# Optimization experiments

Hardware: AMD Instinct MI355X
Metric: run time of the kernel (lower is better)

The kernel has to match this reference:

```python
import jax, jax.numpy as jnp
import numpy as np

DIM_Q = 512
DIM_K = 512
DIM_V = 512
NUM_HEADS = 8
TEMPERATURE = 0.1
LN_EPS = 1e-5


def setup_inputs() -> dict:
    key = jax.random.key(0)
    ks = jax.random.split(key, 12)
    B, n_q, n_k = 8, 1024, 1024
    s = 0.02
    return {
        "Q": jax.random.normal(ks[0], (B, n_q, DIM_Q), jnp.float32),
        "K": jax.random.normal(ks[1], (B, n_k, DIM_K), jnp.float32),
        "mask": jnp.ones((B, n_k), dtype=bool),
        "Wq": jax.random.normal(ks[2], (DIM_Q, DIM_V), jnp.float32) * s,
        "bq": jnp.zeros((DIM_V,), jnp.float32),
        "Wk": jax.random.normal(ks[3], (DIM_K, DIM_V), jnp.float32) * s,
        "bk": jnp.zeros((DIM_V,), jnp.float32),
        "Wv": jax.random.normal(ks[4], (DIM_K, DIM_V), jnp.float32) * s,
        "bv": jnp.zeros((DIM_V,), jnp.float32),
        "Wo": jax.random.normal(ks[5], (DIM_V, DIM_V), jnp.float32) * s,
        "bo": jnp.zeros((DIM_V,), jnp.float32),
        "gamma": jnp.ones((DIM_V,), jnp.float32),
        "beta": jnp.zeros((DIM_V,), jnp.float32),
    }


def _mab(Q, K, mask, Wq, bq, Wk, bk, Wv, bv, Wo, bo, gamma, beta):
    B, n_q, _ = Q.shape
    n_k = K.shape[1]
    H = NUM_HEADS
    d_head = DIM_V // H
    # projections, split heads: [B, H, n, d_head]
    Qh = (Q @ Wq + bq).reshape(B, n_q, H, d_head).transpose(0, 2, 1, 3)
    Kh = (K @ Wk + bk).reshape(B, n_k, H, d_head).transpose(0, 2, 1, 3)
    Vh = (K @ Wv + bv).reshape(B, n_k, H, d_head).transpose(0, 2, 1, 3)
    scale = 1.0 / (np.sqrt(d_head) * TEMPERATURE)
    A = jnp.einsum("bhqd,bhkd->bhqk", Qh, Kh) * scale
    A = jnp.where(mask[:, None, None, :], A, -jnp.inf)
    A = jax.nn.softmax(A, axis=-1)
    O = jnp.einsum("bhqk,bhkd->bhqd", A, Vh)
    O = O.transpose(0, 2, 1, 3).reshape(B, n_q, DIM_V)
    # fused output FFN + residual + LN
    O = O + jax.nn.relu(O @ Wo + bo)
    mu = jnp.mean(O, axis=-1, keepdims=True)
    var = jnp.var(O, axis=-1, keepdims=True)
    return (O - mu) * jax.lax.rsqrt(var + LN_EPS) * gamma + beta


def reference(Q, K, mask, Wq, bq, Wk, bk, Wv, bv, Wo, bo, gamma, beta):
    return _mab(Q, K, mask, Wq, bq, Wk, bk, Wv, bv, Wo, bo, gamma, beta)
```

## Files before the change

### kernel.cpp

```cpp
#include <hip/hip_runtime.h>

typedef __bf16 bf16;
typedef bf16 bf16x4 __attribute__((ext_vector_type(4)));
typedef bf16 bf16x8 __attribute__((ext_vector_type(8)));
typedef float floatx4 __attribute__((ext_vector_type(4)));

#define NB 8
#define NQ 1024
#define NK 1024
#define DIM 512
#define NH 8
#define DH 64

__device__ __forceinline__ void async16(const void* g, void* l) {
    __builtin_amdgcn_global_load_lds(
        (const __attribute__((address_space(1))) unsigned int*)(unsigned long long)(g),
        (__attribute__((address_space(3))) unsigned int*)(unsigned long long)(l),
        16, 0, 0);
}

__global__ __launch_bounds__(256) void prep_fused(
    const float* __restrict__ Q, const float* __restrict__ K,
    const float* __restrict__ Wq, const float* __restrict__ Wk,
    const float* __restrict__ Wv, const float* __restrict__ Wo,
    bf16* __restrict__ Qb, bf16* __restrict__ Kb, bf16* __restrict__ Wt)
{
    __shared__ bf16 Tl[64][68];
    const int bid = blockIdx.x;
    if (bid < 4096) {
        const int i = bid * 256 + threadIdx.x;
        float4 a = ((const float4*)Q)[i];
        float4 c = ((const float4*)K)[i];
        bf16x4 qa = {(bf16)a.x, (bf16)a.y, (bf16)a.z, (bf16)a.w};
        bf16x4 ka = {(bf16)c.x, (bf16)c.y, (bf16)c.z, (bf16)c.w};
        *(bf16x4*)(Qb + (size_t)i * 4) = qa;
        *(bf16x4*)(Kb + (size_t)i * 4) = ka;
    } else {
        const int bid2 = bid - 4096;
        const int w = bid2 >> 6;
        const int bx = bid2 & 7, by = (bid2 >> 3) & 7;
        const float* W = (w == 0) ? Wq : (w == 1) ? Wk : (w == 2) ? Wv : Wo;
        bf16* out = Wt + (size_t)w * DIM * DIM;
        const int k0 = bx * 64, n0 = by * 64;
        const int tx = threadIdx.x & 15, ty = threadIdx.x >> 4;
        for (int pass = 0; pass < 4; ++pass) {
            int k = ty + pass * 16;
            float4 v = *(const float4*)&W[(size_t)(k0 + k) * DIM + n0 + tx * 4];
            Tl[tx * 4 + 0][k] = (bf16)v.x;
            Tl[tx * 4 + 1][k] = (bf16)v.y;
            Tl[tx * 4 + 2][k] = (bf16)v.z;
            Tl[tx * 4 + 3][k] = (bf16)v.w;
        }
        __syncthreads();
        for (int pass = 0; pass < 4; ++pass) {
            int n = ty + pass * 16;
            bf16x4 ov = *(const bf16x4*)&Tl[n][tx * 4];
            *(bf16x4*)&out[(size_t)(n0 + n) * DIM + k0 + tx * 4] = ov;
        }
    }
}

__global__ __launch_bounds__(256) void proj_fused(
    const bf16* __restrict__ Qb, const bf16* __restrict__ Kb,
    const bf16* __restrict__ Wt,
    const float* __restrict__ bq, const float* __restrict__ bk,
    const float* __restrict__ bv,
    bf16* __restrict__ Qp, bf16* __restrict__ Kp, bf16* __restrict__ Vpt)
{
    __shared__ __attribute__((aligned(16))) bf16 sh[16384];
    bf16* As = sh;
    bf16* Bs = sh + 8192;
    const int t = threadIdx.x;
    const int wave = t >> 6, lane = t & 63, quad = lane >> 4, l16 = lane & 15;
    const int wr = wave >> 1, wc = wave & 1;
    const int bid = blockIdx.x;
    const bool isQ = bid < 256;
    const bf16* A; const bf16* W; int m0, n0;
    if (isQ) { A = Qb; W = Wt;             m0 = (bid & 63) * 128;  n0 = (bid >> 6) * 128; }
    else     { int b2 = bid - 256;
               A = Kb; W = Wt + 512 * DIM; m0 = (b2 & 63) * 128;   n0 = (b2 >> 6) * 128; }

    const int r1 = t >> 3, s1 = t & 7;
    const int p1 = s1 ^ (r1 & 7);
    const bf16* aSrc = A + (size_t)(m0 + r1) * DIM + p1 * 8;
    const bf16* wSrc = W + (size_t)(n0 + r1) * DIM + p1 * 8;

    floatx4 acc[4][4];
    for (int i = 0; i < 4; ++i)
        for (int j = 0; j < 4; ++j) acc[i][j] = (floatx4){0.f, 0.f, 0.f, 0.f};

    for (int kt = 0; kt < 8; ++kt) {
        __syncthreads();
        const int ko = kt * 64;
        #pragma unroll
        for (int j = 0; j < 4; ++j) {
            async16(aSrc + ko + (size_t)j * 32 * DIM, As + (t + j * 256) * 8);
            async16(wSrc + ko + (size_t)j * 32 * DIM, Bs + (t + j * 256) * 8);
        }
        __syncthreads();
        #pragma unroll
        for (int ks = 0; ks < 2; ++ks) {
            bf16x8 af[4], bfr[4];
            #pragma unroll
            for (int mi = 0; mi < 4; ++mi) {
                const int row = wr * 64 + mi * 16 + l16;
                af[mi] = *(const bf16x8*)(As + row * 64 + (((ks * 4 + quad) ^ (row & 7)) << 3));
            }
            #pragma unroll
            for (int ni = 0; ni < 4; ++ni) {
                const int row = wc * 64 + ni * 16 + l16;
                bfr[ni] = *(const bf16x8*)(Bs + row * 64 + (((ks * 4 + quad) ^ (row & 7)) << 3));
            }
            #pragma unroll
            for (int mi = 0; mi < 4; ++mi)
                #pragma unroll
                for (int ni = 0; ni < 4; ++ni)
                    acc[mi][ni] = __builtin_amdgcn_mfma_f32_16x16x32_bf16(
                        af[mi], bfr[ni], acc[mi][ni], 0, 0, 0);
        }
    }

    const bool isV = (!isQ) && (n0 >= 512);
    if (!isV) {
        bf16* out = isQ ? Qp : Kp;
        const float* bias = isQ ? bq : bk;
        for (int ni = 0; ni < 4; ++ni) {
            const int n = n0 + wc * 64 + ni * 16 + l16;
            const float bb = bias[n];
            const int hd = n >> 6, d = n & 63;
            for (int mi = 0; mi < 4; ++mi) {
                for (int r = 0; r < 4; ++r) {
                    const int m = m0 + wr * 64 + mi * 16 + quad * 4 + r;
                    const int b = m >> 10, q = m & 1023;
                    out[((size_t)(b * 8 + hd) * 1024 + q) * 64 + d] = (bf16)(acc[mi][ni][r] + bb);
                }
            }
        }
    } else {
        __syncthreads();
        for (int ni = 0; ni < 4; ++ni) {
            const int n = wc * 64 + ni * 16 + l16;
            const float bb = bv[n0 + n - 512];
            for (int mi = 0; mi < 4; ++mi) {
                const int mb = wr * 64 + mi * 16 + quad * 4;
                const int slot = ((mb >> 3) ^ (n & 15));
                bf16x4 pk = {(bf16)(acc[mi][ni][0] + bb), (bf16)(acc[mi][ni][1] + bb),
                             (bf16)(acc[mi][ni][2] + bb), (bf16)(acc[mi][ni][3] + bb)};
                *(bf16x4*)(sh + n * 128 + slot * 8 + (mb & 7)) = pk;
            }
        }
        __syncthreads();
        const int n = t >> 1, hf = t & 1;
        const int nv = n0 + n - 512, hd = nv >> 6, d = nv & 63;
        const int b = m0 >> 10, qb = m0 & 1023;
        bf16* dst = Vpt + ((size_t)(b * 8 + hd) * 64 + d) * 1024 + qb + hf * 64;
        #pragma unroll
        for (int j = 0; j < 8; ++j) {
            const int ch = hf * 8 + j;
            const int slot = ch ^ (n & 15);
            bf16x8 v8 = *(const bf16x8*)(sh + n * 128 + slot * 8);
            *(bf16x8*)(dst + j * 8) = v8;
        }
    }
}

__global__ __launch_bounds__(256) void attn_kernel(
    const bf16* __restrict__ Qp, const bf16* __restrict__ Kp,
    const bf16* __restrict__ Vpt, const int* __restrict__ mask,
    bf16* __restrict__ Oa)
{
    const int bh = blockIdx.x & 63, qblk = blockIdx.x >> 6;
    const int b = bh >> 3, hd = bh & 7;
    const int t = threadIdx.x;
    const int wave = t >> 6, lane = t & 63, quad = lane >> 4, l16 = lane & 15;
    const float scale2 = 1.8033688011112042f;

    __shared__ __attribute__((aligned(16))) bf16 Kt[64 * 64];
    __shared__ __attribute__((aligned(16))) bf16 Vt[64 * 64];
    __shared__ __attribute__((aligned(16))) bf16 Pl[4][16 * 64];

    const bf16* Qbase = Qp + ((size_t)bh * NQ + qblk * 64 + wave * 16) * DH;
    const bf16* Kbase = Kp + (size_t)bh * NK * DH;
    const bf16* Vbase = Vpt + (size_t)bh * DH * NK;
    const int* mrow = mask + b * NK;

    bf16x8 qf[2];
    for (int hh = 0; hh < 2; ++hh)
        qf[hh] = *(const bf16x8*)(Qbase + l16 * DH + hh * 32 + quad * 8);

    floatx4 o[4];
    float lsum = 0.f;
    for (int i = 0; i < 4; ++i) o[i] = (floatx4){0.f, 0.f, 0.f, 0.f};

    const int r1 = t >> 3, s1 = t & 7;
    const int p1 = s1 ^ (r1 & 7);
    const bf16* kSrc = Kbase + r1 * 64 + p1 * 8;
    const bf16* vSrc = Vbase + (size_t)r1 * 1024 + p1 * 8;
    bf16* kDst0 = Kt + t * 8;
    bf16* kDst1 = Kt + (t + 256) * 8;
    bf16* vDst0 = Vt + t * 8;
    bf16* vDst1 = Vt + (t + 256) * 8;

    for (int kt = 0; kt < NK / 64; ++kt) {
        __syncthreads();
        async16(kSrc + kt * 4096, kDst0);
        async16(kSrc + kt * 4096 + 32 * 64, kDst1);
        async16(vSrc + kt * 64, vDst0);
        async16(vSrc + kt * 64 + (size_t)32 * 1024, vDst1);
        __syncthreads();

        bf16x8 kb[4][2];
        #pragma unroll
        for (int sub = 0; sub < 4; ++sub) {
            const int rowk = sub * 16 + l16;
            kb[sub][0] = *(const bf16x8*)(Kt + rowk * 64 + ((quad ^ (rowk & 7)) << 3));
            kb[sub][1] = *(const bf16x8*)(Kt + rowk * 64 + (((quad + 4) ^ (rowk & 7)) << 3));
        }
        floatx4 sf[4];
        #pragma unroll
        for (int sub = 0; sub < 4; ++sub) {
            floatx4 s = {0.f, 0.f, 0.f, 0.f};
            s = __builtin_amdgcn_mfma_f32_16x16x32_bf16(kb[sub][0], qf[0], s, 0, 0, 0);
            s = __builtin_amdgcn_mfma_f32_16x16x32_bf16(kb[sub][1], qf[1], s, 0, 0, 0);
            sf[sub] = s;
        }
        #pragma unroll
        for (int sub = 0; sub < 4; ++sub) {
            const int4 m4 = *(const int4*)&mrow[kt * 64 + sub * 16 + quad * 4];
            const float md0 = m4.x ? 0.f : -3.0e38f;
            const float md1 = m4.y ? 0.f : -3.0e38f;
            const float md2 = m4.z ? 0.f : -3.0e38f;
            const float md3 = m4.w ? 0.f : -3.0e38f;
            float p0 = exp2f(fmaf(sf[sub][0], scale2, md0));
            float p1v = exp2f(fmaf(sf[sub][1], scale2, md1));
            float p2 = exp2f(fmaf(sf[sub][2], scale2, md2));
            float p3 = exp2f(fmaf(sf[sub][3], scale2, md3));
            sf[sub][0] = p0; sf[sub][1] = p1v; sf[sub][2] = p2; sf[sub][3] = p3;
            lsum += p0 + p1v + p2 + p3;
        }
        #pragma unroll
        for (int sub = 0; sub < 4; ++sub) {
            bf16x4 pk = {(bf16)sf[sub][0], (bf16)sf[sub][1],
                         (bf16)sf[sub][2], (bf16)sf[sub][3]};
            const int p = sub * 2 + (quad >> 1);
            const int slot = p ^ (l16 & 7);
            *(bf16x4*)&Pl[wave][l16 * 64 + slot * 8 + (quad & 1) * 4] = pk;
        }
        bf16x8 af[2];
        #pragma unroll
        for (int hh = 0; hh < 2; ++hh) {
            const int p = hh * 4 + quad;
            const int slot = p ^ (l16 & 7);
            af[hh] = *(const bf16x8*)&Pl[wave][l16 * 64 + slot * 8];
        }
        #pragma unroll
        for (int dsub = 0; dsub < 4; ++dsub) {
            const int rowd = dsub * 16 + l16;
            bf16x8 v0 = *(const bf16x8*)(Vt + rowd * 64 + ((quad ^ (rowd & 7)) << 3));
            bf16x8 v1 = *(const bf16x8*)(Vt + rowd * 64 + (((quad + 4) ^ (rowd & 7)) << 3));
            o[dsub] = __builtin_amdgcn_mfma_f32_16x16x32_bf16(af[0], v0, o[dsub], 0, 0, 0);
            o[dsub] = __builtin_amdgcn_mfma_f32_16x16x32_bf16(af[1], v1, o[dsub], 0, 0, 0);
        }
    }

    float lr = lsum;
    lr += __shfl_xor(lr, 16, 64);
    lr += __shfl_xor(lr, 32, 64);
    const float inv = 1.f / lr;
    float linv[4];
    for (int r = 0; r < 4; ++r) linv[r] = __shfl(inv, quad * 4 + r, 64);
    for (int dsub = 0; dsub < 4; ++dsub) {
        for (int r = 0; r < 4; ++r) {
            const int q = qblk * 64 + wave * 16 + quad * 4 + r;
            const int col = hd * 64 + dsub * 16 + l16;
            Oa[((size_t)(b * NQ + q)) * DIM + col] = (bf16)(o[dsub][r] * linv[r]);
        }
    }
}

__global__ __launch_bounds__(256) void ffn_ln(
    const bf16* __restrict__ Oa, const bf16* __restrict__ W,
    const float* __restrict__ bo, const float* __restrict__ gamma,
    const float* __restrict__ beta, float* __restrict__ out)
{
    __shared__ __attribute__((aligned(16))) bf16 As[32 * 512];
    __shared__ __attribute__((aligned(16))) bf16 Bs[512 * 32];
    const int t = threadIdx.x;
    const int wave = t >> 6, lane = t & 63, quad = lane >> 4, l16 = lane & 15;
    const int m0 = blockIdx.x * 32;

    #pragma unroll
    for (int j = 0; j < 8; ++j) {
        const int c = t + j * 256;
        const int row = c >> 6, slot = c & 63;
        const int p = (slot & 56) | ((slot & 7) ^ (row & 7));
        async16(Oa + (size_t)(m0 + row) * DIM + p * 8, As + row * 512 + slot * 8);
    }

    floatx4 acc[2][8];
    for (int i = 0; i < 2; ++i)
        for (int j = 0; j < 8; ++j) acc[i][j] = (floatx4){0.f, 0.f, 0.f, 0.f};

    for (int kt = 0; kt < 16; ++kt) {
        __syncthreads();
        #pragma unroll
        for (int j = 0; j < 8; ++j) {
            const int c = t + j * 256;
            const int n = c >> 2, slot = c & 3;
            const int p = slot ^ ((n >> 1) & 3);
            async16(W + (size_t)n * DIM + kt * 32 + p * 8, Bs + n * 32 + slot * 8);
        }
        __syncthreads();
        bf16x8 af[2], bfr[8];
        #pragma unroll
        for (int mi = 0; mi < 2; ++mi) {
            const int row = mi * 16 + l16;
            const int part = kt * 4 + quad;
            const int slot = (part & 56) | ((part & 7) ^ (row & 7));
            af[mi] = *(const bf16x8*)(As + row * 512 + slot * 8);
        }
        #pragma unroll
        for (int ni = 0; ni < 8; ++ni) {
            const int n = wave * 128 + ni * 16 + l16;
            const int slot = quad ^ ((n >> 1) & 3);
            bfr[ni] = *(const bf16x8*)(Bs + n * 32 + slot * 8);
        }
        #pragma unroll
        for (int mi = 0; mi < 2; ++mi)
            #pragma unroll
            for (int ni = 0; ni < 8; ++ni)
                acc[mi][ni] = __builtin_amdgcn_mfma_f32_16x16x32_bf16(
                    af[mi], bfr[ni], acc[mi][ni], 0, 0, 0);
    }

    #pragma unroll
    for (int ni = 0; ni < 8; ++ni) {
        const int n = wave * 128 + ni * 16 + l16;
        const float bb = bo[n];
        const int part = n >> 3, noff = n & 7;
        #pragma unroll
        for (int mi = 0; mi < 2; ++mi) {
            #pragma unroll
            for (int r = 0; r < 4; ++r) {
                const int row = mi * 16 + quad * 4 + r;
                const int slot = (part & 56) | ((part & 7) ^ (row & 7));
                const float res = (float)As[row * 512 + slot * 8 + noff];
                acc[mi][ni][r] = res + fmaxf(acc[mi][ni][r] + bb, 0.f);
            }
        }
    }

    __syncthreads();
    float* Sm  = (float*)Bs;
    float* Sq  = Sm + 128;
    float* Mu  = Sm + 256;
    float* Inv = Sm + 288;
    #pragma unroll
    for (int mi = 0; mi < 2; ++mi) {
        #pragma unroll
        for (int r = 0; r < 4; ++r) {
            float s = 0.f, q2 = 0.f;
            #pragma unroll
            for (int ni = 0; ni < 8; ++ni) {
                const float v = acc[mi][ni][r];
                s += v; q2 += v * v;
            }
            s  += __shfl_xor(s, 1, 64);  q2 += __shfl_xor(q2, 1, 64);
            s  += __shfl_xor(s, 2, 64);  q2 += __shfl_xor(q2, 2, 64);
            s  += __shfl_xor(s, 4, 64);  q2 += __shfl_xor(q2, 4, 64);
            s  += __shfl_xor(s, 8, 64);  q2 += __shfl_xor(q2, 8, 64);
            if (l16 == 0) {
                const int row = mi * 16 + quad * 4 + r;
                Sm[wave * 32 + row] = s;
                Sq[wave * 32 + row] = q2;
            }
        }
    }
    __syncthreads();
    if (t < 32) {
        const float s  = Sm[t] + Sm[32 + t] + Sm[64 + t] + Sm[96 + t];
        const float q2 = Sq[t] + Sq[32 + t] + Sq[64 + t] + Sq[96 + t];
        const float mu = s * (1.f / 512.f);
        const float var = q2 * (1.f / 512.f) - mu * mu;
        Mu[t] = mu;
        Inv[t] = rsqrtf(var + 1e-5f);
    }
    __syncthreads();

    #pragma unroll
    for (int ni = 0; ni < 8; ++ni) {
        const int n = wave * 128 + ni * 16 + l16;
        const float gv = gamma[n], btv = beta[n];
        #pragma unroll
        for (int mi = 0; mi < 2; ++mi) {
            #pragma unroll
            for (int r = 0; r < 4; ++r) {
                const int row = mi * 16 + quad * 4 + r;
                const float mu = Mu[row], iv = Inv[row];
                out[(size_t)(m0 + row) * DIM + n] =
                    (acc[mi][ni][r] - mu) * iv * gv + btv;
            }
        }
    }
}

extern "C" void kernel_launch(void* const* d_in, const int* in_sizes, int n_in,
                              void* d_out, int out_size, void* d_ws, size_t ws_size,
                              hipStream_t stream) {
    const float* Q  = (const float*)d_in[0];
    const float* K  = (const float*)d_in[1];
    const int*   mask = (const int*)d_in[2];
    const float* Wq = (const float*)d_in[3];
    const float* bq = (const float*)d_in[4];
    const float* Wk = (const float*)d_in[5];
    const float* bk = (const float*)d_in[6];
    const float* Wv = (const float*)d_in[7];
    const float* bv = (const float*)d_in[8];
    const float* Wo = (const float*)d_in[9];
    const float* bo = (const float*)d_in[10];
    const float* gamma = (const float*)d_in[11];
    const float* beta  = (const float*)d_in[12];

    char* ws = (char*)d_ws;
    bf16* Wt  = (bf16*)(ws);
    bf16* Qb  = (bf16*)(ws + 2097152);
    bf16* Kb  = (bf16*)(ws + 10485760);
    bf16* Qp  = (bf16*)(ws + 18874368);
    bf16* Kp  = (bf16*)(ws + 27262976);
    bf16* Vpt = (bf16*)(ws + 35651584);
    bf16* Oa  = (bf16*)(ws + 44040192);
    float* out = (float*)d_out;

    prep_fused<<<4352, 256, 0, stream>>>(Q, K, Wq, Wk, Wv, Wo, Qb, Kb, Wt);
    proj_fused<<<768, 256, 0, stream>>>(Qb, Kb, Wt, bq, bk, bv, Qp, Kp, Vpt);
    attn_kernel<<<1024, 256, 0, stream>>>(Qp, Kp, Vpt, mask, Oa);
    ffn_ln<<<256, 256, 0, stream>>>(Oa, Wt + 3 * 262144, bo, gamma, beta, out);
}
```

Baseline: 186.9 us.

## Give attention waves two query groups each and halve FFN row tile

The attention kernel now runs 2 waves per block instead of 4. Each wave handles two 16-row query groups, so every K and V fragment loaded from LDS feeds twice as many MFMAs, and exp2 with a prescale is replaced by __expf with scale 1.25. The FFN+LayerNorm kernel processes 16 rows per block instead of 32, doubling the grid to 512 blocks for better occupancy. The tradeoffs are more registers per attention wave and more redundant reloads of Wo per row in the FFN.

```diff
diff --git a/kernel.cpp b/kernel.cpp
--- a/kernel.cpp
+++ b/kernel.cpp
@@ -164,7 +164,7 @@
     }
 }
 
-__global__ __launch_bounds__(256) void attn_kernel(
+__global__ __launch_bounds__(128) void attn_kernel(
     const bf16* __restrict__ Qp, const bf16* __restrict__ Kp,
     const bf16* __restrict__ Vpt, const int* __restrict__ mask,
     bf16* __restrict__ Oa)
@@ -173,40 +173,41 @@
     const int b = bh >> 3, hd = bh & 7;
     const int t = threadIdx.x;
     const int wave = t >> 6, lane = t & 63, quad = lane >> 4, l16 = lane & 15;
-    const float scale2 = 1.8033688011112042f;
+    const float scale = 1.25f;
 
     __shared__ __attribute__((aligned(16))) bf16 Kt[64 * 64];
     __shared__ __attribute__((aligned(16))) bf16 Vt[64 * 64];
-    __shared__ __attribute__((aligned(16))) bf16 Pl[4][16 * 64];
-
-    const bf16* Qbase = Qp + ((size_t)bh * NQ + qblk * 64 + wave * 16) * DH;
+    __shared__ __attribute__((aligned(16))) bf16 Pl[2][32 * 64];
+
+    const bf16* Qbase = Qp + ((size_t)bh * NQ + qblk * 64 + wave * 32) * DH;
     const bf16* Kbase = Kp + (size_t)bh * NK * DH;
     const bf16* Vbase = Vpt + (size_t)bh * DH * NK;
     const int* mrow = mask + b * NK;
 
-    bf16x8 qf[2];
-    for (int hh = 0; hh < 2; ++hh)
-        qf[hh] = *(const bf16x8*)(Qbase + l16 * DH + hh * 32 + quad * 8);
-
-    floatx4 o[4];
-    float lsum = 0.f;
-    for (int i = 0; i < 4; ++i) o[i] = (floatx4){0.f, 0.f, 0.f, 0.f};
+    bf16x8 qf[2][2];
+    for (int g = 0; g < 2; ++g)
+        for (int hh = 0; hh < 2; ++hh)
+            qf[g][hh] = *(const bf16x8*)(Qbase + (g * 16 + l16) * DH + hh * 32 + quad * 8);
+
+    floatx4 o[2][4];
+    float lsum[2];
+    for (int g = 0; g < 2; ++g) {
+        lsum[g] = 0.f;
+        for (int i = 0; i < 4; ++i) o[g][i] = (floatx4){0.f, 0.f, 0.f, 0.f};
+    }
 
     const int r1 = t >> 3, s1 = t & 7;
     const int p1 = s1 ^ (r1 & 7);
     const bf16* kSrc = Kbase + r1 * 64 + p1 * 8;
     const bf16* vSrc = Vbase + (size_t)r1 * 1024 + p1 * 8;
-    bf16* kDst0 = Kt + t * 8;
-    bf16* kDst1 = Kt + (t + 256) * 8;
-    bf16* vDst0 = Vt + t * 8;
-    bf16* vDst1 = Vt + (t + 256) * 8;
 
     for (int kt = 0; kt < NK / 64; ++kt) {
         __syncthreads();
-        async16(kSrc + kt * 4096, kDst0);
-        async16(kSrc + kt * 4096 + 32 * 64, kDst1);
-        async16(vSrc + kt * 64, vDst0);
-        async16(vSrc + kt * 64 + (size_t)32 * 1024, vDst1);
+        #pragma unroll
+        for (int j = 0; j < 4; ++j) {
+            async16(kSrc + kt * 4096 + j * 16 * 64, Kt + (t + j * 128) * 8);
+            async16(vSrc + kt * 64 + (size_t)j * 16 * 1024, Vt + (t + j * 128) * 8);
+        }
         __syncthreads();
 
         bf16x8 kb[4][2];
@@ -216,14 +217,16 @@
             kb[sub][0] = *(const bf16x8*)(Kt + rowk * 64 + ((quad ^ (rowk & 7)) << 3));
             kb[sub][1] = *(const bf16x8*)(Kt + rowk * 64 + (((quad + 4) ^ (rowk & 7)) << 3));
         }
-        floatx4 sf[4];
-        #pragma unroll
-        for (int sub = 0; sub < 4; ++sub) {
-            floatx4 s = {0.f, 0.f, 0.f, 0.f};
-            s = __builtin_amdgcn_mfma_f32_16x16x32_bf16(kb[sub][0], qf[0], s, 0, 0, 0);
-            s = __builtin_amdgcn_mfma_f32_16x16x32_bf16(kb[sub][1], qf[1], s, 0, 0, 0);
-            sf[sub] = s;
-        }
+        floatx4 sf[2][4];
+        #pragma unroll
+        for (int g = 0; g < 2; ++g)
+            #pragma unroll
+            for (int sub = 0; sub < 4; ++sub) {
+                floatx4 s = {0.f, 0.f, 0.f, 0.f};
+                s = __builtin_amdgcn_mfma_f32_16x16x32_bf16(kb[sub][0], qf[g][0], s, 0, 0, 0);
+                s = __builtin_amdgcn_mfma_f32_16x16x32_bf16(kb[sub][1], qf[g][1], s, 0, 0, 0);
+                sf[g][sub] = s;
+            }
         #pragma unroll
         for (int sub = 0; sub < 4; ++sub) {
             const int4 m4 = *(const int4*)&mrow[kt * 64 + sub * 16 + quad * 4];
@@ -231,49 +234,60 @@
             const float md1 = m4.y ? 0.f : -3.0e38f;
             const float md2 = m4.z ? 0.f : -3.0e38f;
             const float md3 = m4.w ? 0.f : -3.0e38f;
-            float p0 = exp2f(fmaf(sf[sub][0], scale2, md0));
-            float p1v = exp2f(fmaf(sf[sub][1], scale2, md1));
-            float p2 = exp2f(fmaf(sf[sub][2], scale2, md2));
-            float p3 = exp2f(fmaf(sf[sub][3], scale2, md3));
-            sf[sub][0] = p0; sf[sub][1] = p1v; sf[sub][2] = p2; sf[sub][3] = p3;
-            lsum += p0 + p1v + p2 + p3;
-        }
-        #pragma unroll
-        for (int sub = 0; sub < 4; ++sub) {
-            bf16x4 pk = {(bf16)sf[sub][0], (bf16)sf[sub][1],
-                         (bf16)sf[sub][2], (bf16)sf[sub][3]};
-            const int p = sub * 2 + (quad >> 1);
-            const int slot = p ^ (l16 & 7);
-            *(bf16x4*)&Pl[wave][l16 * 64 + slot * 8 + (quad & 1) * 4] = pk;
-        }
-        bf16x8 af[2];
-        #pragma unroll
-        for (int hh = 0; hh < 2; ++hh) {
-            const int p = hh * 4 + quad;
-            const int slot = p ^ (l16 & 7);
-            af[hh] = *(const bf16x8*)&Pl[wave][l16 * 64 + slot * 8];
-        }
+            #pragma unroll
+            for (int g = 0; g < 2; ++g) {
+                float p0 = __expf(sf[g][sub][0] * scale + md0);
+                float p1v = __expf(sf[g][sub][1] * scale + md1);
+                float p2 = __expf(sf[g][sub][2] * scale + md2);
+                float p3 = __expf(sf[g][sub][3] * scale + md3);
+                sf[g][sub][0] = p0; sf[g][sub][1] = p1v;
+                sf[g][sub][2] = p2; sf[g][sub][3] = p3;
+                lsum[g] += p0 + p1v + p2 + p3;
+            }
+        }
+        #pragma unroll
+        for (int g = 0; g < 2; ++g)
+            #pragma unroll
+            for (int sub = 0; sub < 4; ++sub) {
+                bf16x4 pk = {(bf16)sf[g][sub][0], (bf16)sf[g][sub][1],
+                             (bf16)sf[g][sub][2], (bf16)sf[g][sub][3]};
+                const int slot = (sub * 2 + (quad >> 1)) ^ (l16 & 7);
+                *(bf16x4*)&Pl[wave][(g * 16 + l16) * 64 + slot * 8 + (quad & 1) * 4] = pk;
+            }
+        bf16x8 af[2][2];
+        #pragma unroll
+        for (int g = 0; g < 2; ++g)
+            #pragma unroll
+            for (int hh = 0; hh < 2; ++hh) {
+                const int slot = (hh * 4 + quad) ^ (l16 & 7);
+                af[g][hh] = *(const bf16x8*)&Pl[wave][(g * 16 + l16) * 64 + slot * 8];
+            }
         #pragma unroll
         for (int dsub = 0; dsub < 4; ++dsub) {
             const int rowd = dsub * 16 + l16;
             bf16x8 v0 = *(const bf16x8*)(Vt + rowd * 64 + ((quad ^ (rowd & 7)) << 3));
             bf16x8 v1 = *(const bf16x8*)(Vt + rowd * 64 + (((quad + 4) ^ (rowd & 7)) << 3));
-            o[dsub] = __builtin_amdgcn_mfma_f32_16x16x32_bf16(af[0], v0, o[dsub], 0, 0, 0);
-            o[dsub] = __builtin_amdgcn_mfma_f32_16x16x32_bf16(af[1], v1, o[dsub], 0, 0, 0);
-        }
-    }
-
-    float lr = lsum;
-    lr += __shfl_xor(lr, 16, 64);
-    lr += __shfl_xor(lr, 32, 64);
-    const float inv = 1.f / lr;
-    float linv[4];
-    for (int r = 0; r < 4; ++r) linv[r] = __shfl(inv, quad * 4 + r, 64);
-    for (int dsub = 0; dsub < 4; ++dsub) {
-        for (int r = 0; r < 4; ++r) {
-            const int q = qblk * 64 + wave * 16 + quad * 4 + r;
-            const int col = hd * 64 + dsub * 16 + l16;
-            Oa[((size_t)(b * NQ + q)) * DIM + col] = (bf16)(o[dsub][r] * linv[r]);
+            #pragma unroll
+            for (int g = 0; g < 2; ++g) {
+                o[g][dsub] = __builtin_amdgcn_mfma_f32_16x16x32_bf16(af[g][0], v0, o[g][dsub], 0, 0, 0);
+                o[g][dsub] = __builtin_amdgcn_mfma_f32_16x16x32_bf16(af[g][1], v1, o[g][dsub], 0, 0, 0);
+            }
+        }
+    }
+
+    for (int g = 0; g < 2; ++g) {
+        float lr = lsum[g];
+        lr += __shfl_xor(lr, 16, 64);
+        lr += __shfl_xor(lr, 32, 64);
+        const float inv = 1.f / lr;
+        float linv[4];
+        for (int r = 0; r < 4; ++r) linv[r] = __shfl(inv, quad * 4 + r, 64);
+        for (int dsub = 0; dsub < 4; ++dsub) {
+            for (int r = 0; r < 4; ++r) {
+                const int q = qblk * 64 + wave * 32 + g * 16 + quad * 4 + r;
+                const int col = hd * 64 + dsub * 16 + l16;
+                Oa[((size_t)(b * NQ + q)) * DIM + col] = (bf16)(o[g][dsub][r] * linv[r]);
+            }
         }
     }
 }
@@ -283,23 +297,22 @@
     const float* __restrict__ bo, const float* __restrict__ gamma,
     const float* __restrict__ beta, float* __restrict__ out)
 {
-    __shared__ __attribute__((aligned(16))) bf16 As[32 * 512];
+    __shared__ __attribute__((aligned(16))) bf16 As[16 * 512];
     __shared__ __attribute__((aligned(16))) bf16 Bs[512 * 32];
     const int t = threadIdx.x;
     const int wave = t >> 6, lane = t & 63, quad = lane >> 4, l16 = lane & 15;
-    const int m0 = blockIdx.x * 32;
+    const int m0 = blockIdx.x * 16;
 
     #pragma unroll
-    for (int j = 0; j < 8; ++j) {
+    for (int j = 0; j < 4; ++j) {
         const int c = t + j * 256;
         const int row = c >> 6, slot = c & 63;
         const int p = (slot & 56) | ((slot & 7) ^ (row & 7));
         async16(Oa + (size_t)(m0 + row) * DIM + p * 8, As + row * 512 + slot * 8);
     }
 
-    floatx4 acc[2][8];
-    for (int i = 0; i < 2; ++i)
-        for (int j = 0; j < 8; ++j) acc[i][j] = (floatx4){0.f, 0.f, 0.f, 0.f};
+    floatx4 acc[8];
+    for (int j = 0; j < 8; ++j) acc[j] = (floatx4){0.f, 0.f, 0.f, 0.f};
 
     for (int kt = 0; kt < 16; ++kt) {
         __syncthreads();
@@ -311,13 +324,11 @@
             async16(W + (size_t)n * DIM + kt * 32 + p * 8, Bs + n * 32 + slot * 8);
         }
         __syncthreads();
-        bf16x8 af[2], bfr[8];
-        #pragma unroll
-        for (int mi = 0; mi < 2; ++mi) {
-            const int row = mi * 16 + l16;
+        bf16x8 af, bfr[8];
+        {
             const int part = kt * 4 + quad;
-            const int slot = (part & 56) | ((part & 7) ^ (row & 7));
-            af[mi] = *(const bf16x8*)(As + row * 512 + slot * 8);
+            const int slot = (part & 56) | ((part & 7) ^ (l16 & 7));
+            af = *(const bf16x8*)(As + l16 * 512 + slot * 8);
         }
         #pragma unroll
         for (int ni = 0; ni < 8; ++ni) {
@@ -326,11 +337,8 @@
             bfr[ni] = *(const bf16x8*)(Bs + n * 32 + slot * 8);
         }
         #pragma unroll
-        for (int mi = 0; mi < 2; ++mi)
-            #pragma unroll
-            for (int ni = 0; ni < 8; ++ni)
-                acc[mi][ni] = __builtin_amdgcn_mfma_f32_16x16x32_bf16(
-                    af[mi], bfr[ni], acc[mi][ni], 0, 0, 0);
+        for (int ni = 0; ni < 8; ++ni)
+            acc[ni] = __builtin_amdgcn_mfma_f32_16x16x32_bf16(af, bfr[ni], acc[ni], 0, 0, 0);
     }
 
     #pragma unroll
@@ -339,47 +347,41 @@
         const float bb = bo[n];
         const int part = n >> 3, noff = n & 7;
         #pragma unroll
-        for (int mi = 0; mi < 2; ++mi) {
-            #pragma unroll
-            for (int r = 0; r < 4; ++r) {
-                const int row = mi * 16 + quad * 4 + r;
-                const int slot = (part & 56) | ((part & 7) ^ (row & 7));
-                const float res = (float)As[row * 512 + slot * 8 + noff];
-                acc[mi][ni][r] = res + fmaxf(acc[mi][ni][r] + bb, 0.f);
-            }
+        for (int r = 0; r < 4; ++r) {
+            const int row = quad * 4 + r;
+            const int slot = (part & 56) | ((part & 7) ^ (row & 7));
+            const float res = (float)As[row * 512 + slot * 8 + noff];
+            acc[ni][r] = res + fmaxf(acc[ni][r] + bb, 0.f);
         }
     }
 
     __syncthreads();
     float* Sm  = (float*)Bs;
-    float* Sq  = Sm + 128;
-    float* Mu  = Sm + 256;
-    float* Inv = Sm + 288;
+    float* Sq  = Sm + 64;
+    float* Mu  = Sm + 128;
+    float* Inv = Sm + 144;
     #pragma unroll
-    for (int mi = 0; mi < 2; ++mi) {
-        #pragma unroll
-        for (int r = 0; r < 4; ++r) {
-            float s = 0.f, q2 = 0.f;
-            #pragma unroll
-            for (int ni = 0; ni < 8; ++ni) {
-                const float v = acc[mi][ni][r];
-                s += v; q2 += v * v;
-            }
-            s  += __shfl_xor(s, 1, 64);  q2 += __shfl_xor(q2, 1, 64);
-            s  += __shfl_xor(s, 2, 64);  q2 += __shfl_xor(q2, 2, 64);
-            s  += __shfl_xor(s, 4, 64);  q2 += __shfl_xor(q2, 4, 64);
-            s  += __shfl_xor(s, 8, 64);  q2 += __shfl_xor(q2, 8, 64);
-            if (l16 == 0) {
-                const int row = mi * 16 + quad * 4 + r;
-                Sm[wave * 32 + row] = s;
-                Sq[wave * 32 + row] = q2;
-            }
+    for (int r = 0; r < 4; ++r) {
+        float s = 0.f, q2 = 0.f;
+        #pragma unroll
+        for (int ni = 0; ni < 8; ++ni) {
+            const float v = acc[ni][r];
+            s += v; q2 += v * v;
+        }
+        s  += __shfl_xor(s, 1, 64);  q2 += __shfl_xor(q2, 1, 64);
+        s  += __shfl_xor(s, 2, 64);  q2 += __shfl_xor(q2, 2, 64);
+        s  += __shfl_xor(s, 4, 64);  q2 += __shfl_xor(q2, 4, 64);
+        s  += __shfl_xor(s, 8, 64);  q2 += __shfl_xor(q2, 8, 64);
+        if (l16 == 0) {
+            const int row = quad * 4 + r;
+            Sm[wave * 16 + row] = s;
+            Sq[wave * 16 + row] = q2;
         }
     }
     __syncthreads();
-    if (t < 32) {
-        const float s  = Sm[t] + Sm[32 + t] + Sm[64 + t] + Sm[96 + t];
-        const float q2 = Sq[t] + Sq[32 + t] + Sq[64 + t] + Sq[96 + t];
+    if (t < 16) {
+        const float s  = Sm[t] + Sm[16 + t] + Sm[32 + t] + Sm[48 + t];
+        const float q2 = Sq[t] + Sq[16 + t] + Sq[32 + t] + Sq[48 + t];
         const float mu = s * (1.f / 512.f);
         const float var = q2 * (1.f / 512.f) - mu * mu;
         Mu[t] = mu;
@@ -392,14 +394,10 @@
         const int n = wave * 128 + ni * 16 + l16;
         const float gv = gamma[n], btv = beta[n];
         #pragma unroll
-        for (int mi = 0; mi < 2; ++mi) {
-            #pragma unroll
-            for (int r = 0; r < 4; ++r) {
-                const int row = mi * 16 + quad * 4 + r;
-                const float mu = Mu[row], iv = Inv[row];
-                out[(size_t)(m0 + row) * DIM + n] =
-                    (acc[mi][ni][r] - mu) * iv * gv + btv;
-            }
+        for (int r = 0; r < 4; ++r) {
+            const int row = quad * 4 + r;
+            out[(size_t)(m0 + row) * DIM + n] =
+                (acc[ni][r] - Mu[row]) * Inv[row] * gv + btv;
         }
     }
 }
@@ -433,6 +431,6 @@
 
     prep_fused<<<4352, 256, 0, stream>>>(Q, K, Wq, Wk, Wv, Wo, Qb, Kb, Wt);
     proj_fused<<<768, 256, 0, stream>>>(Qb, Kb, Wt, bq, bk, bv, Qp, Kp, Vpt);
-    attn_kernel<<<1024, 256, 0, stream>>>(Qp, Kp, Vpt, mask, Oa);
-    ffn_ln<<<256, 256, 0, stream>>>(Oa, Wt + 3 * 262144, bo, gamma, beta, out);
-}
+    attn_kernel<<<1024, 128, 0, stream>>>(Qp, Kp, Vpt, mask, Oa);
+    ffn_ln<<<512, 256, 0, stream>>>(Oa, Wt + 3 * 262144, bo, gamma, beta, out);
+}
```

Result: slower. 197.0 us (+5.4%).
